# Optimization experiments

Hardware: AMD Instinct MI355X
Metric: run time of the kernel (lower is better)

The kernel has to match this reference:

```python
import jax, jax.numpy as jnp
import numpy as np

DIM = 1024
N_HEADS = 16
HEAD_DIM = DIM // N_HEADS
ROPE_BASE = 10000.0


def setup_inputs() -> dict:
    key = jax.random.key(0)
    ks = jax.random.split(key, 5)
    B, T = 4, 2048
    s_in = 1.0 / np.sqrt(DIM)
    x = jax.random.normal(ks[0], (B, T, DIM), dtype=jnp.float32)
    W_qkv = jax.random.uniform(ks[1], (DIM, 3 * DIM), jnp.float32, -s_in, s_in)
    b_qkv = jax.random.uniform(ks[2], (3 * DIM,), jnp.float32, -s_in, s_in)
    W_proj = jax.random.uniform(ks[3], (DIM, DIM), jnp.float32, -s_in, s_in)
    b_proj = jax.random.uniform(ks[4], (DIM,), jnp.float32, -s_in, s_in)
    return {"x": x, "W_qkv": W_qkv, "b_qkv": b_qkv, "W_proj": W_proj, "b_proj": b_proj}


def _rope_cos_sin(T, dtype):
    inv_freq = 1.0 / (ROPE_BASE ** (jnp.arange(0, HEAD_DIM, 2, dtype=jnp.float32) / HEAD_DIM))
    t = jnp.arange(T, dtype=jnp.float32)
    freqs = jnp.outer(t, inv_freq)            # (T, HEAD_DIM/2)
    emb = jnp.concatenate([freqs, freqs], -1)  # (T, HEAD_DIM)
    return jnp.cos(emb).astype(dtype), jnp.sin(emb).astype(dtype)


def _rotate_half(x):
    x1, x2 = jnp.split(x, 2, axis=-1)
    return jnp.concatenate([-x2, x1], axis=-1)


def reference(x, W_qkv, b_qkv, W_proj, b_proj):
    B, T, C = x.shape
    qkv = x @ W_qkv + b_qkv                              # (B, T, 3C)
    qkv = qkv.reshape(B, T, 3, N_HEADS, HEAD_DIM)
    qkv = jnp.transpose(qkv, (2, 0, 3, 1, 4))            # (3, B, H, T, d)
    q, k, v = qkv[0], qkv[1], qkv[2]
    cos, sin = _rope_cos_sin(T, x.dtype)
    cos = cos[None, None]                                # (1,1,T,d)
    sin = sin[None, None]
    q = q * cos + _rotate_half(q) * sin
    k = k * cos + _rotate_half(k) * sin
    scale = 1.0 / np.sqrt(HEAD_DIM)
    scores = jnp.einsum('bhqd,bhkd->bhqk', q, k) * scale  # (B,H,T,T)
    attn = jax.nn.softmax(scores, axis=-1)
    out = jnp.einsum('bhqk,bhkd->bhqd', attn, v)          # (B,H,T,d)
    out = jnp.transpose(out, (0, 2, 1, 3)).reshape(B, T, C)
    return out @ W_proj + b_proj
```

## Files before the change

### kernel.cpp

```cpp
#include <hip/hip_runtime.h>
#include <hip/hip_bf16.h>
#include <cstdint>
#include <cstddef>

typedef __bf16 bf16x8 __attribute__((ext_vector_type(8)));
typedef float f32x4 __attribute__((ext_vector_type(4)));
typedef float f32x16 __attribute__((ext_vector_type(16)));
typedef unsigned short ushort8 __attribute__((ext_vector_type(8)));

#define MFMA16(a, b, c) __builtin_amdgcn_mfma_f32_16x16x32_bf16(a, b, c, 0, 0, 0)
#define MFMA32(a, b, c) __builtin_amdgcn_mfma_f32_32x32x16_bf16(a, b, c, 0, 0, 0)

__device__ __forceinline__ void gll16(const void* g, void* l) {
  __builtin_amdgcn_global_load_lds((__attribute__((address_space(1))) unsigned int*)g,
                                   (__attribute__((address_space(3))) unsigned int*)l,
                                   16, 0, 0);
}

__device__ __forceinline__ float exp2_raw(float x) {
  return __builtin_amdgcn_exp2f(x);
}

__device__ __forceinline__ bf16x8 pack8(float a0, float a1, float a2, float a3,
                                        float a4, float a5, float a6, float a7) {
  unsigned w0, w1, w2, w3;
  asm("v_cvt_pk_bf16_f32 %0, %1, %2" : "=v"(w0) : "v"(a0), "v"(a1));
  asm("v_cvt_pk_bf16_f32 %0, %1, %2" : "=v"(w1) : "v"(a2), "v"(a3));
  asm("v_cvt_pk_bf16_f32 %0, %1, %2" : "=v"(w2) : "v"(a4), "v"(a5));
  asm("v_cvt_pk_bf16_f32 %0, %1, %2" : "=v"(w3) : "v"(a6), "v"(a7));
  asm("v_permlane32_swap_b32 %0, %1" : "+v"(w0), "+v"(w2));
  asm("v_permlane32_swap_b32 %0, %1" : "+v"(w1), "+v"(w3));
  union { unsigned u[4]; bf16x8 v; } r;
  r.u[0] = w0; r.u[1] = w1; r.u[2] = w2; r.u[3] = w3;
  return r.v;
}


__global__ void cvt_x(const float* __restrict__ in, __bf16* __restrict__ out) {
  int i = (blockIdx.x * 256 + threadIdx.x) * 8;
  float4 a = *(const float4*)(in + i);
  float4 c = *(const float4*)(in + i + 4);
  bf16x8 r;
  r[0] = (__bf16)a.x; r[1] = (__bf16)a.y; r[2] = (__bf16)a.z; r[3] = (__bf16)a.w;
  r[4] = (__bf16)c.x; r[5] = (__bf16)c.y; r[6] = (__bf16)c.z; r[7] = (__bf16)c.w;
  *(bf16x8*)(out + i) = r;
}

__global__ void rope_tab_k(float2* __restrict__ tab) {
  int i = blockIdx.x * 256 + threadIdx.x;
  int t = i >> 5, ii = i & 31;
  float invf = exp2f(-(float)ii * (13.287712379549449f / 32.0f));
  float a = (float)t * invf;
  tab[i] = make_float2(cosf(a), sinf(a));
}

__global__ void transp_bf16(const float* __restrict__ W, __bf16* __restrict__ Wt,
                            int K, int N) {
  __shared__ float tile[32][33];
  int n0 = blockIdx.x * 32, k0 = blockIdx.y * 32;
  int tx = threadIdx.x & 31, ty = threadIdx.x >> 5;
  #pragma unroll
  for (int r = ty; r < 32; r += 8)
    tile[r][tx] = W[(size_t)(k0 + r) * N + n0 + tx];
  __syncthreads();
  #pragma unroll
  for (int r = ty; r < 32; r += 8)
    Wt[(size_t)(n0 + r) * K + k0 + tx] = (__bf16)tile[tx][r];
}

__global__ void transp_v(const __bf16* __restrict__ in, __bf16* __restrict__ out) {
  __shared__ unsigned short tile[64][72];
  const int bh = blockIdx.y, t0 = blockIdx.x * 64;
  const int tid = threadIdx.x;
  const int r = tid >> 3, c = (tid & 7) * 8;
  const __bf16* src = in + ((size_t)bh * 2048 + t0) * 64;
  ushort8 a = *(const ushort8*)(src + (size_t)r * 64 + c);
  ushort8 b = *(const ushort8*)(src + (size_t)(r + 32) * 64 + c);
  #pragma unroll
  for (int e = 0; e < 8; ++e) { tile[c + e][r] = a[e]; tile[c + e][r + 32] = b[e]; }
  __syncthreads();
  const int d = tid >> 3, tc = tid & 7;
  __bf16* dst0 = out + ((size_t)bh * 64 + d) * 2048 + t0;
  *(ushort8*)(dst0 + tc * 8) = *(const ushort8*)&tile[d][tc * 8];
  __bf16* dst1 = out + ((size_t)bh * 64 + d + 32) * 2048 + t0;
  *(ushort8*)(dst1 + tc * 8) = *(const ushort8*)&tile[d + 32][tc * 8];
}

template <int EPI>
__global__ __launch_bounds__(256, 2) void gemm_bt(
    const __bf16* __restrict__ A, const __bf16* __restrict__ Bt,
    const float* __restrict__ bias, float* __restrict__ Cf,
    __bf16* __restrict__ qp, __bf16* __restrict__ kp, __bf16* __restrict__ vp,
    const float2* __restrict__ ctab, int M, int N, int K) {
  __shared__ __align__(16) char smem[32768];
  const int tid = threadIdx.x;
  const int w = tid >> 6, l = tid & 63, l15 = l & 15, g = l >> 4;
  const int wr = w >> 1, wc = w & 1;
  const int brow = blockIdx.y * 128, bcol = blockIdx.x * 128;

  f32x4 acc[4][4] = {};
  const int rsub = tid >> 3;
  const int csub = (tid & 7) * 16;

  for (int kt = 0; kt < K; kt += 64) {
    __syncthreads();
    #pragma unroll
    for (int i = 0; i < 4; ++i) {
      const char* ga = (const char*)(A + (size_t)(brow + i * 32 + rsub) * K + kt) + csub;
      gll16(ga, smem + i * 4096 + tid * 16);
      const char* gb = (const char*)(Bt + (size_t)(bcol + i * 32 + rsub) * K + kt) + csub;
      gll16(gb, smem + 16384 + i * 4096 + tid * 16);
    }
    __syncthreads();
    #pragma unroll
    for (int kk = 0; kk < 2; ++kk) {
      bf16x8 af[4], bfr[4];
      #pragma unroll
      for (int m = 0; m < 4; ++m)
        af[m] = *(const bf16x8*)(smem + (wr * 64 + m * 16 + l15) * 128 + kk * 64 + g * 16);
      #pragma unroll
      for (int n = 0; n < 4; ++n)
        bfr[n] = *(const bf16x8*)(smem + 16384 + (wc * 64 + n * 16 + l15) * 128 + kk * 64 + g * 16);
      #pragma unroll
      for (int m = 0; m < 4; ++m)
        #pragma unroll
        for (int n = 0; n < 4; ++n)
          acc[m][n] = MFMA16(af[m], bfr[n], acc[m][n]);
    }
  }

  const int colb = bcol + wc * 64;
  float bs[4];
  #pragma unroll
  for (int n = 0; n < 4; ++n) bs[n] = bias[colb + n * 16 + l15];

  if (EPI == 1) {
    #pragma unroll
    for (int m = 0; m < 4; ++m)
      #pragma unroll
      for (int j = 0; j < 4; ++j) {
        int row = brow + wr * 64 + m * 16 + g * 4 + j;
        float* crow = Cf + (size_t)row * N + colb;
        #pragma unroll
        for (int n = 0; n < 4; ++n)
          crow[n * 16 + l15] = acc[m][n][j] + bs[n];
      }
  } else {
    const int which = colb >> 10;
    const int h = (colb & 1023) >> 6;
    __bf16* dst = (which == 0) ? qp : (which == 1) ? kp : vp;
    const float SCLQ = 0.18033688011112042f;
    #pragma unroll
    for (int m = 0; m < 4; ++m)
      #pragma unroll
      for (int j = 0; j < 4; ++j) {
        int row = brow + wr * 64 + m * 16 + g * 4 + j;
        int bb = row >> 11, t = row & 2047;
        float v0 = acc[m][0][j] + bs[0];
        float v1 = acc[m][1][j] + bs[1];
        float v2 = acc[m][2][j] + bs[2];
        float v3 = acc[m][3][j] + bs[3];
        if (which < 2) {
          float2 cs0 = ctab[t * 32 + l15];
          float2 cs1 = ctab[t * 32 + 16 + l15];
          float r0 = v0 * cs0.x - v2 * cs0.y;
          float r2 = v2 * cs0.x + v0 * cs0.y;
          float r1 = v1 * cs1.x - v3 * cs1.y;
          float r3 = v3 * cs1.x + v1 * cs1.y;
          v0 = r0; v1 = r1; v2 = r2; v3 = r3;
        }
        if (which == 0) { v0 *= SCLQ; v1 *= SCLQ; v2 *= SCLQ; v3 *= SCLQ; }
        __bf16* orow = dst + ((size_t)(bb * 16 + h) * 2048 + t) * 64;
        orow[l15]      = (__bf16)v0;
        orow[16 + l15] = (__bf16)v1;
        orow[32 + l15] = (__bf16)v2;
        orow[48 + l15] = (__bf16)v3;
      }
  }
}

__global__ __launch_bounds__(256, 4) void flash_attn(
    const __bf16* __restrict__ q, const __bf16* __restrict__ k,
    const __bf16* __restrict__ vt, __bf16* __restrict__ o) {
  __shared__ __align__(16) char smem[32768];
  const int id = blockIdx.x;
  const int nid = (id & 7) * 128 + (id >> 3);
  const int bh = nid >> 4, qb = nid & 15;
  const int b = bh >> 4, h = bh & 15;
  const int tid = threadIdx.x, w = tid >> 6, l = tid & 63;
  const int l31 = l & 31, hi = l >> 5;

  const char* kbase  = (const char*)(k  + (size_t)bh * 2048 * 64);
  const char* vtbase = (const char*)(vt + (size_t)bh * 64 * 2048);

  bf16x8 qf[4];
  const int qrow0 = qb * 128 + w * 32;
  #pragma unroll
  for (int ks = 0; ks < 4; ++ks)
    qf[ks] = *(const bf16x8*)(q + (size_t)bh * 2048 * 64 +
                              (size_t)(qrow0 + l31) * 64 + ks * 16 + hi * 8);

  f32x16 accO[2] = {};
  float lr = 0.f;

  const int koff[2] = { 0, 16384 };
  const int voff[2] = { 8192, 24576 };

  const int srow = tid >> 3;
  const int ssw  = (((tid & 7) ^ ((tid >> 3) & 7) ^ (((tid >> 6) & 3) << 1)) << 4);
  const int swz  = (((l & 7) ^ (((l >> 3) & 3) << 1)) << 4);

  gll16(kbase + srow * 128 + ssw,                  smem + koff[0] + tid * 16);
  gll16(kbase + (srow + 32) * 128 + ssw,           smem + koff[0] + 4096 + tid * 16);
  gll16(vtbase + (size_t)srow * 4096 + ssw,        smem + voff[0] + tid * 16);
  gll16(vtbase + (size_t)(srow + 32) * 4096 + ssw, smem + voff[0] + 4096 + tid * 16);
  __syncthreads();

  for (int t = 0; t < 32; ++t) {
    const int cur = t & 1;
    char* Kc = smem + koff[cur];
    char* Vc = smem + voff[cur];
    if (t < 31) {
      char* Kn = smem + koff[cur ^ 1];
      char* Vn = smem + voff[cur ^ 1];
      const char* gk = kbase + (size_t)(t + 1) * 8192;
      gll16(gk + srow * 128 + ssw,        Kn + tid * 16);
      gll16(gk + (srow + 32) * 128 + ssw, Kn + 4096 + tid * 16);
      const char* gv = vtbase + (size_t)(t + 1) * 128;
      gll16(gv + (size_t)srow * 4096 + ssw,        Vn + tid * 16);
      gll16(gv + (size_t)(srow + 32) * 4096 + ssw, Vn + 4096 + tid * 16);
    }

    f32x16 st0 = {}, st1 = {};
    __builtin_amdgcn_s_setprio(1);
    #pragma unroll
    for (int ks = 0; ks < 4; ++ks) {
      bf16x8 kf0 = *(const bf16x8*)(Kc + (l31) * 128 + ((ks * 32 + hi * 16) ^ swz));
      bf16x8 kf1 = *(const bf16x8*)(Kc + (32 + l31) * 128 + ((ks * 32 + hi * 16) ^ swz));
      st0 = MFMA32(kf0, qf[ks], st0);
      st1 = MFMA32(kf1, qf[ks], st1);
    }
    __builtin_amdgcn_s_setprio(0);

    bf16x8 pa[4];
    {
      float p[16];
      #pragma unroll
      for (int r = 0; r < 16; ++r) p[r] = exp2_raw(st0[r]);
      lr += (((p[0] + p[1]) + (p[2] + p[3])) + ((p[4] + p[5]) + (p[6] + p[7]))) +
            (((p[8] + p[9]) + (p[10] + p[11])) + ((p[12] + p[13]) + (p[14] + p[15])));
      pa[0] = pack8(p[0], p[1], p[2], p[3], p[4], p[5], p[6], p[7]);
      pa[1] = pack8(p[8], p[9], p[10], p[11], p[12], p[13], p[14], p[15]);
    }
    {
      float p[16];
      #pragma unroll
      for (int r = 0; r < 16; ++r) p[r] = exp2_raw(st1[r]);
      lr += (((p[0] + p[1]) + (p[2] + p[3])) + ((p[4] + p[5]) + (p[6] + p[7]))) +
            (((p[8] + p[9]) + (p[10] + p[11])) + ((p[12] + p[13]) + (p[14] + p[15])));
      pa[2] = pack8(p[0], p[1], p[2], p[3], p[4], p[5], p[6], p[7]);
      pa[3] = pack8(p[8], p[9], p[10], p[11], p[12], p[13], p[14], p[15]);
    }

    __builtin_amdgcn_s_setprio(1);
    #pragma unroll
    for (int ks = 0; ks < 4; ++ks) {
      bf16x8 vf0 = *(const bf16x8*)(Vc + (l31) * 128 + ((ks * 32 + hi * 16) ^ swz));
      bf16x8 vf1 = *(const bf16x8*)(Vc + (32 + l31) * 128 + ((ks * 32 + hi * 16) ^ swz));
      accO[0] = MFMA32(pa[ks], vf0, accO[0]);
      accO[1] = MFMA32(pa[ks], vf1, accO[1]);
    }
    __builtin_amdgcn_s_setprio(0);
    __syncthreads();
  }

  float lrf = lr + __shfl_xor(lr, 32);
  __bf16* obase = o + (size_t)(b * 2048) * 1024 + h * 64;
  #pragma unroll
  for (int r = 0; r < 16; ++r) {
    int qloc = (r & 3) + 8 * (r >> 2) + 4 * hi;
    float inv = 1.0f / __shfl(lrf, qloc);
    __bf16* orow = obase + (size_t)(qrow0 + qloc) * 1024;
    orow[l31]      = (__bf16)(accO[0][r] * inv);
    orow[32 + l31] = (__bf16)(accO[1][r] * inv);
  }
}


extern "C" void kernel_launch(void* const* d_in, const int* in_sizes, int n_in,
                              void* d_out, int out_size, void* d_ws, size_t ws_size,
                              hipStream_t stream) {
  const float* x     = (const float*)d_in[0];
  const float* Wqkv  = (const float*)d_in[1];
  const float* bqkv  = (const float*)d_in[2];
  const float* Wproj = (const float*)d_in[3];
  const float* bproj = (const float*)d_in[4];
  float* out = (float*)d_out;

  char* ws = (char*)d_ws;
  __bf16* xb  = (__bf16*)(ws);
  __bf16* wtq = (__bf16*)(ws + 16777216);
  __bf16* wtp = (__bf16*)(ws + 23068672);
  __bf16* qp  = (__bf16*)(ws + 25165824);
  __bf16* kp  = (__bf16*)(ws + 41943040);
  __bf16* vp  = (__bf16*)(ws + 58720256);
  __bf16* ao  = (__bf16*)(ws + 75497472);
  float2* ct  = (float2*)(ws + 92274688);
  __bf16* vtp = xb;
  if (ws_size < 92798976) return;

  cvt_x<<<4096, 256, 0, stream>>>(x, xb);
  rope_tab_k<<<256, 256, 0, stream>>>(ct);
  transp_bf16<<<dim3(96, 32), 256, 0, stream>>>(Wqkv, wtq, 1024, 3072);
  transp_bf16<<<dim3(32, 32), 256, 0, stream>>>(Wproj, wtp, 1024, 1024);
  gemm_bt<0><<<dim3(24, 64), 256, 0, stream>>>(xb, wtq, bqkv, nullptr, qp, kp, vp, ct,
                                               8192, 3072, 1024);
  transp_v<<<dim3(32, 64), 256, 0, stream>>>(vp, vtp);
  flash_attn<<<1024, 256, 0, stream>>>(qp, kp, vtp, ao);
  gemm_bt<1><<<dim3(8, 64), 256, 0, stream>>>(ao, wtp, bproj, out, nullptr, nullptr,
                                              nullptr, nullptr, 8192, 1024, 1024);
}
```

Baseline: 208.2 us.

## Rewrite GEMMs with 256x128 tiles, triple-buffered async LDS loads and swizzling

Replaces the 128x128 single-buffered GEMM with a 512-thread, 256x128-tile kernel that prefetches two K-tiles ahead into a three-stage LDS ring using global_load_lds and explicit vmcnt waits. LDS chunks are XOR-swizzled to avoid bank conflicts, and MFMA sections are raised in priority. This aims to overlap global loads with MFMA compute and improve data reuse. In exchange it needs 144KB of dynamic LDS, which limits blocks per CU, and halves the number of blocks in the grid.

Measured after the change: 208.9 us. About the same (+0.4%).

```diff
diff --git a/kernel.cpp b/kernel.cpp
--- a/kernel.cpp
+++ b/kernel.cpp
@@ -87,49 +87,98 @@
 }
 
 template <int EPI>
-__global__ __launch_bounds__(256, 2) void gemm_bt(
+__global__ __launch_bounds__(512, 2) void gemm256(
     const __bf16* __restrict__ A, const __bf16* __restrict__ Bt,
     const float* __restrict__ bias, float* __restrict__ Cf,
     __bf16* __restrict__ qp, __bf16* __restrict__ kp, __bf16* __restrict__ vp,
     const float2* __restrict__ ctab, int M, int N, int K) {
-  __shared__ __align__(16) char smem[32768];
+  extern __shared__ __align__(16) char smem[];
   const int tid = threadIdx.x;
   const int w = tid >> 6, l = tid & 63, l15 = l & 15, g = l >> 4;
-  const int wr = w >> 1, wc = w & 1;
-  const int brow = blockIdx.y * 128, bcol = blockIdx.x * 128;
+  const int wm = w >> 1, wn = w & 1;
+  const int brow = blockIdx.y * 256, bcol = blockIdx.x * 128;
+  const int NT = K >> 6;
+
+  const int srow = tid >> 3;
+  const int sf   = ((srow & 7) ^ (((srow >> 3) & 3) << 1));
+  const int schunk = (((tid & 7) ^ sf) << 4);
+
+  int frx[4];
+  #pragma unroll
+  for (int x = 0; x < 4; ++x)
+    frx[x] = ((l15 & 7) ^ (((2 * x + (l15 >> 3)) & 3) << 1));
 
   f32x4 acc[4][4] = {};
-  const int rsub = tid >> 3;
-  const int csub = (tid & 7) * 16;
-
-  for (int kt = 0; kt < K; kt += 64) {
-    __syncthreads();
-    #pragma unroll
-    for (int i = 0; i < 4; ++i) {
-      const char* ga = (const char*)(A + (size_t)(brow + i * 32 + rsub) * K + kt) + csub;
-      gll16(ga, smem + i * 4096 + tid * 16);
-      const char* gb = (const char*)(Bt + (size_t)(bcol + i * 32 + rsub) * K + kt) + csub;
-      gll16(gb, smem + 16384 + i * 4096 + tid * 16);
-    }
-    __syncthreads();
-    #pragma unroll
-    for (int kk = 0; kk < 2; ++kk) {
-      bf16x8 af[4], bfr[4];
-      #pragma unroll
-      for (int m = 0; m < 4; ++m)
-        af[m] = *(const bf16x8*)(smem + (wr * 64 + m * 16 + l15) * 128 + kk * 64 + g * 16);
-      #pragma unroll
-      for (int n = 0; n < 4; ++n)
-        bfr[n] = *(const bf16x8*)(smem + 16384 + (wc * 64 + n * 16 + l15) * 128 + kk * 64 + g * 16);
+
+  const size_t rowK2 = (size_t)K * 2;
+  #pragma unroll
+  for (int t = 0; t < 2; ++t) {
+    char* Ab = smem + t * 49152;
+    char* Bb = Ab + 32768;
+    const char* As = (const char*)A + ((size_t)(brow + srow) * K + t * 64) * 2 + schunk;
+    #pragma unroll
+    for (int i = 0; i < 4; ++i)
+      gll16(As + (size_t)i * 64 * rowK2, Ab + i * 8192 + tid * 16);
+    const char* Bs = (const char*)Bt + ((size_t)(bcol + srow) * K + t * 64) * 2 + schunk;
+    #pragma unroll
+    for (int i = 0; i < 2; ++i)
+      gll16(Bs + (size_t)i * 64 * rowK2, Bb + i * 8192 + tid * 16);
+  }
+
+  for (int kt = 0; kt < NT; ++kt) {
+    asm volatile("" ::: "memory");
+    __builtin_amdgcn_s_barrier();
+    asm volatile("" ::: "memory");
+
+    if (kt + 2 < NT) {
+      const int t = kt + 2, buf = t % 3;
+      char* Ab = smem + buf * 49152;
+      char* Bb = Ab + 32768;
+      const char* As = (const char*)A + ((size_t)(brow + srow) * K + t * 64) * 2 + schunk;
+      #pragma unroll
+      for (int i = 0; i < 4; ++i)
+        gll16(As + (size_t)i * 64 * rowK2, Ab + i * 8192 + tid * 16);
+      const char* Bs = (const char*)Bt + ((size_t)(bcol + srow) * K + t * 64) * 2 + schunk;
+      #pragma unroll
+      for (int i = 0; i < 2; ++i)
+        gll16(Bs + (size_t)i * 64 * rowK2, Bb + i * 8192 + tid * 16);
+    }
+
+    if (kt < NT - 2)       asm volatile("s_waitcnt vmcnt(12)" ::: "memory");
+    else if (kt == NT - 2) asm volatile("s_waitcnt vmcnt(6)" ::: "memory");
+    else                   asm volatile("s_waitcnt vmcnt(0)" ::: "memory");
+
+    asm volatile("" ::: "memory");
+    __builtin_amdgcn_s_barrier();
+    asm volatile("" ::: "memory");
+
+    const char* Ab = smem + (kt % 3) * 49152;
+    const char* Bb = Ab + 32768;
+    bf16x8 af[4][2], bfr[4][2];
+    #pragma unroll
+    for (int m = 0; m < 4; ++m)
+      #pragma unroll
+      for (int kk = 0; kk < 2; ++kk)
+        af[m][kk] = *(const bf16x8*)(Ab + (wm * 64 + m * 16 + l15) * 128 +
+                                     (((kk * 4 + g) ^ frx[m]) << 4));
+    #pragma unroll
+    for (int n = 0; n < 4; ++n)
+      #pragma unroll
+      for (int kk = 0; kk < 2; ++kk)
+        bfr[n][kk] = *(const bf16x8*)(Bb + (wn * 64 + n * 16 + l15) * 128 +
+                                      (((kk * 4 + g) ^ frx[n]) << 4));
+    __builtin_amdgcn_s_setprio(1);
+    #pragma unroll
+    for (int kk = 0; kk < 2; ++kk)
       #pragma unroll
       for (int m = 0; m < 4; ++m)
         #pragma unroll
         for (int n = 0; n < 4; ++n)
-          acc[m][n] = MFMA16(af[m], bfr[n], acc[m][n]);
-    }
-  }
-
-  const int colb = bcol + wc * 64;
+          acc[m][n] = MFMA16(af[m][kk], bfr[n][kk], acc[m][n]);
+    __builtin_amdgcn_s_setprio(0);
+  }
+
+  const int colb = bcol + wn * 64;
   float bs[4];
   #pragma unroll
   for (int n = 0; n < 4; ++n) bs[n] = bias[colb + n * 16 + l15];
@@ -139,7 +188,7 @@
     for (int m = 0; m < 4; ++m)
       #pragma unroll
       for (int j = 0; j < 4; ++j) {
-        int row = brow + wr * 64 + m * 16 + g * 4 + j;
+        int row = brow + wm * 64 + m * 16 + g * 4 + j;
         float* crow = Cf + (size_t)row * N + colb;
         #pragma unroll
         for (int n = 0; n < 4; ++n)
@@ -154,7 +203,7 @@
     for (int m = 0; m < 4; ++m)
       #pragma unroll
       for (int j = 0; j < 4; ++j) {
-        int row = brow + wr * 64 + m * 16 + g * 4 + j;
+        int row = brow + wm * 64 + m * 16 + g * 4 + j;
         int bb = row >> 11, t = row & 2047;
         float v0 = acc[m][0][j] + bs[0];
         float v1 = acc[m][1][j] + bs[1];
@@ -309,14 +358,21 @@
   __bf16* vtp = xb;
   if (ws_size < 92798976) return;
 
+  const int LDS_BYTES = 147456;
+  hipFuncSetAttribute((const void*)gemm256<0>,
+                      hipFuncAttributeMaxDynamicSharedMemorySize, LDS_BYTES);
+  hipFuncSetAttribute((const void*)gemm256<1>,
+                      hipFuncAttributeMaxDynamicSharedMemorySize, LDS_BYTES);
+
   cvt_x<<<4096, 256, 0, stream>>>(x, xb);
   rope_tab_k<<<256, 256, 0, stream>>>(ct);
   transp_bf16<<<dim3(96, 32), 256, 0, stream>>>(Wqkv, wtq, 1024, 3072);
   transp_bf16<<<dim3(32, 32), 256, 0, stream>>>(Wproj, wtp, 1024, 1024);
-  gemm_bt<0><<<dim3(24, 64), 256, 0, stream>>>(xb, wtq, bqkv, nullptr, qp, kp, vp, ct,
-                                               8192, 3072, 1024);
+  gemm256<0><<<dim3(24, 32), 512, LDS_BYTES, stream>>>(xb, wtq, bqkv, nullptr,
+                                                       qp, kp, vp, ct, 8192, 3072, 1024);
   transp_v<<<dim3(32, 64), 256, 0, stream>>>(vp, vtp);
   flash_attn<<<1024, 256, 0, stream>>>(qp, kp, vtp, ao);
-  gemm_bt<1><<<dim3(8, 64), 256, 0, stream>>>(ao, wtp, bproj, out, nullptr, nullptr,
-                                              nullptr, nullptr, 8192, 1024, 1024);
-}
+  gemm256<1><<<dim3(8, 32), 512, LDS_BYTES, stream>>>(ao, wtp, bproj, out,
+                                                      nullptr, nullptr, nullptr, nullptr,
+                                                      8192, 1024, 1024);
+}
```
